# Optimization experiments

Hardware: AMD Instinct MI355X
Metric: run time of the kernel (lower is better)

Reference implementation:

```python
import jax, jax.numpy as jnp
from jax import lax
import numpy as np

N, T, V = 32, 32, 128
C_FEAT, C_BOX, C_CLS = 256, 4, 4
C_IN = C_FEAT + C_BOX + C_CLS  # 264 (is_scene=False concatenates x,b,c)
C_OUT = 64
K = 9
EPS = 1e-3  # keras BatchNormalization default epsilon


def _bn4(x, g, b, m, v):
    # inference-mode BN over channel axis 1 of (N,C,T,V)
    s = (g * lax.rsqrt(v + EPS))[None, :, None, None]
    return (x - m[None, :, None, None]) * s + b[None, :, None, None]


def _stgcn(x, a, imp, w, bw, ga, ba, ma, va, al, wt, bt, gb, bb, mb, vb, residual):
    res = x if residual else 0.0
    # SGCN: 1x1 conv (channels_first) then adjacency aggregation; dropout is identity at inference
    h = jnp.einsum('nctv,co->notv', x, w) + bw[None, :, None, None]
    h = jnp.einsum('nctv,ntvw->nctw', h, a * imp)
    # TGCN: BN -> PReLU(alpha per (C,T,V)) -> temporal conv (K,1) SAME -> BN -> (dropout=id)
    h = _bn4(h, ga, ba, ma, va)
    h = jnp.where(h >= 0, h, al[None] * h)
    h = lax.conv_general_dilated(h, wt, (1, 1), 'SAME',
                                 dimension_numbers=('NCHW', 'HWIO', 'NCHW')) + bt[None, :, None, None]
    h = _bn4(h, gb, bb, mb, vb)
    return h + res  # use_mdn=True -> no final PReLU


def _forward(x, b, c, a, dbn_g, dbn_b, dbn_m, dbn_v,
             w0, bw0, imp0, g0a, b0a, m0a, v0a, al0, wt0, bt0, g0b, b0b, m0b, v0b,
             w1, bw1, imp1, g1a, b1a, m1a, v1a, al1, wt1, bt1, g1b, b1b, m1b, v1b):
    x = jnp.concatenate([x, b, c], axis=-1)  # (N,T,V,C_IN)
    n, t, v, cc = x.shape
    # data BN over flattened (V*C) channel axis, exactly as the TF reshapes do
    x = jnp.transpose(x, (0, 2, 3, 1)).reshape(n, v * cc, t)
    s = (dbn_g * lax.rsqrt(dbn_v + EPS))[None, :, None]
    x = (x - dbn_m[None, :, None]) * s + dbn_b[None, :, None]
    # NOTE: the original does transpose(0,1,3,2) then a *reshape* to (N,C,T,V); replicate exactly
    x = x.reshape(n, v, cc, t).transpose(0, 1, 3, 2).reshape(n, cc, t, v)
    x = _stgcn(x, a, imp0, w0, bw0, g0a, b0a, m0a, v0a, al0, wt0, bt0, g0b, b0b, m0b, v0b, residual=False)
    x = _stgcn(x, a, imp1, w1, bw1, g1a, b1a, m1a, v1a, al1, wt1, bt1, g1b, b1b, m1b, v1b, residual=True)
    x = x[:, :, :, 0]  # (N,C_OUT,T)
    return jnp.transpose(x, (0, 2, 1))  # (N,T,C_OUT)


def setup_inputs():
    key = jax.random.key(0)
    ks = jax.random.split(key, 40)
    rn = lambda k, s, sc=1.0: jax.random.normal(k, s, jnp.float32) * sc
    ru = lambda k, s, lo, hi: jax.random.uniform(k, s, jnp.float32, lo, hi)
    d = {}
    d['x'] = rn(ks[0], (N, T, V, C_FEAT))
    d['b'] = rn(ks[1], (N, T, V, C_BOX))
    d['c'] = ru(ks[2], (N, T, V, C_CLS), 0.0, 1.0)
    d['a'] = ru(ks[3], (N, T, V, V), 0.0, 1.0)
    d['dbn_g'] = ru(ks[4], (V * C_IN,), 0.5, 1.5)
    d['dbn_b'] = rn(ks[5], (V * C_IN,), 0.1)
    d['dbn_m'] = rn(ks[6], (V * C_IN,), 0.1)
    d['dbn_v'] = ru(ks[7], (V * C_IN,), 0.5, 1.5)

    def mk_layer(i, cin, kb):
        d['w%d' % i] = rn(ks[kb], (cin, C_OUT), (1.0 / cin) ** 0.5)
        d['bw%d' % i] = rn(ks[kb + 1], (C_OUT,), 0.01)
        d['imp%d' % i] = rn(ks[kb + 2], (V, V), (2.0 / (V * V)) ** 0.5)
        d['g%da' % i] = ru(ks[kb + 3], (C_OUT,), 0.5, 1.5)
        d['b%da' % i] = rn(ks[kb + 4], (C_OUT,), 0.1)
        d['m%da' % i] = rn(ks[kb + 5], (C_OUT,), 0.1)
        d['v%da' % i] = ru(ks[kb + 6], (C_OUT,), 0.5, 1.5)
        d['al%d' % i] = ru(ks[kb + 7], (C_OUT, T, V), 0.0, 0.3)
        d['wt%d' % i] = rn(ks[kb + 8], (K, 1, C_OUT, C_OUT), (1.0 / (K * C_OUT)) ** 0.5)
        d['bt%d' % i] = rn(ks[kb + 9], (C_OUT,), 0.01)
        d['g%db' % i] = ru(ks[kb + 10], (C_OUT,), 0.5, 1.5)
        d['b%db' % i] = rn(ks[kb + 11], (C_OUT,), 0.1)
        d['m%db' % i] = rn(ks[kb + 12], (C_OUT,), 0.1)
        d['v%db' % i] = ru(ks[kb + 13], (C_OUT,), 0.5, 1.5)

    mk_layer(0, C_IN, 8)
    mk_layer(1, C_OUT, 22)
    return d


def reference(x, b, c, a, dbn_g, dbn_b, dbn_m, dbn_v,
              w0, bw0, imp0, g0a, b0a, m0a, v0a, al0, wt0, bt0, g0b, b0b, m0b, v0b,
              w1, bw1, imp1, g1a, b1a, m1a, v1a, al1, wt1, bt1, g1b, b1b, m1b, v1b):
    return _forward(x, b, c, a, dbn_g, dbn_b, dbn_m, dbn_v,
                    w0, bw0, imp0, g0a, b0a, m0a, v0a, al0, wt0, bt0, g0b, b0b, m0b, v0b,
                    w1, bw1, imp1, g1a, b1a, m1a, v1a, al1, wt1, bt1, g1b, b1b, m1b, v1b)
```

## Files before the change

kernel.cpp:

```cpp
#include <hip/hip_runtime.h>
#include <hip/hip_bf16.h>

typedef unsigned short u16;
typedef unsigned int   u32;

#define N_   32
#define T_   32
#define V_   128
#define CIN_ 264
#define CO_  64
#define KT_  9
#define EPS_ 1e-3f

#define OFF_DBN_S 0
#define OFF_DBN_O 33792
#define OFF_W0    67584
#define OFF_BW0   84480
#define OFF_A0S   84544
#define OFF_A0O   84608
#define OFF_B0S   84672
#define OFF_B0O   84736
#define OFF_W1    84800
#define OFF_BW1   88896
#define OFF_A1S   88960
#define OFF_A1O   89024
#define OFF_B1S   89088
#define OFF_B1O   89152
#define PREP_TOTAL 110464

#define B_P    0
#define B_FLAG 360448
#define B_W0A  360512
#define B_WTA  397440
#define B_H0   524288
#define B_XP   (B_H0 + 16777216)
#define B_G0   (B_H0 + 16777216)
#define B_L0   (B_G0 + 16777216)
#define B_G1P  (B_L0 + 33554432)
#define B_END  (B_G1P + 262144)

typedef short bf16x8 __attribute__((ext_vector_type(8)));
typedef float f32x4  __attribute__((ext_vector_type(4)));

__device__ __forceinline__ float bf2f(u16 u) { return __uint_as_float(((u32)u) << 16); }
__device__ __forceinline__ u16 f2bf(float f) {
    u32 x = __float_as_uint(f);
    return (u16)((x + 0x7fffu + ((x >> 16) & 1u)) >> 16);
}
__device__ __forceinline__ float ldin(const void* p, u32 i, int f32) {
    return f32 ? ((const float*)p)[i] : bf2f(((const u16*)p)[i]);
}

__global__ void k_detect(const void* a, int* flag) {
    if (threadIdx.x == 0 && blockIdx.x == 0) {
        const u16* p = (const u16*)a;
        int cnt = 0;
        for (int i = 0; i < 64; ++i) {
            float v = bf2f(p[2 * i]);
            if (v >= 0.f && v <= 1.0f) ++cnt;
        }
        *flag = (cnt >= 56) ? 0 : 1;
    }
}

__global__ void k_prep(const void* dbn_g, const void* dbn_b, const void* dbn_m, const void* dbn_v,
                       const void* w0, const void* bw0,
                       const void* g0a, const void* b0a, const void* m0a, const void* v0a,
                       const void* bt0, const void* g0b, const void* b0b, const void* m0b, const void* v0b,
                       const void* w1, const void* bw1,
                       const void* g1a, const void* b1a, const void* m1a, const void* v1a,
                       const void* bt1, const void* g1b, const void* b1b, const void* m1b, const void* v1b,
                       const void* wt0,
                       float* P, u16* W0A, u16* WTA, const int* flagp)
{
    const int f32 = *flagp;
    int i = blockIdx.x * 256 + threadIdx.x;
    if (i < 33792) {
        float s = ldin(dbn_g, i, f32) * rsqrtf(ldin(dbn_v, i, f32) + EPS_);
        P[OFF_DBN_S + i] = s;
        P[OFF_DBN_O + i] = ldin(dbn_b, i, f32) - ldin(dbn_m, i, f32) * s;
    } else if (i < 50688) { int j = i - 33792; P[OFF_W0 + j] = ldin(w0, j, f32); }
    else if (i < 50752) { int j = i - 50688; P[OFF_BW0 + j] = ldin(bw0, j, f32); }
    else if (i < 50816) { int j = i - 50752;
        float s = ldin(g0a, j, f32) * rsqrtf(ldin(v0a, j, f32) + EPS_);
        P[OFF_A0S + j] = s; P[OFF_A0O + j] = ldin(b0a, j, f32) - ldin(m0a, j, f32) * s;
    } else if (i < 50880) { int j = i - 50816;
        float s = ldin(g0b, j, f32) * rsqrtf(ldin(v0b, j, f32) + EPS_);
        P[OFF_B0S + j] = s; P[OFF_B0O + j] = (ldin(bt0, j, f32) - ldin(m0b, j, f32)) * s + ldin(b0b, j, f32);
    } else if (i < 54976) { int j = i - 50880; P[OFF_W1 + j] = ldin(w1, j, f32); }
    else if (i < 55040) { int j = i - 54976; P[OFF_BW1 + j] = ldin(bw1, j, f32); }
    else if (i < 55104) { int j = i - 55040;
        float s = ldin(g1a, j, f32) * rsqrtf(ldin(v1a, j, f32) + EPS_);
        P[OFF_A1S + j] = s; P[OFF_A1O + j] = ldin(b1a, j, f32) - ldin(m1a, j, f32) * s;
    } else if (i < 55168) { int j = i - 55104;
        float s = ldin(g1b, j, f32) * rsqrtf(ldin(v1b, j, f32) + EPS_);
        P[OFF_B1S + j] = s; P[OFF_B1O + j] = (ldin(bt1, j, f32) - ldin(m1b, j, f32)) * s + ldin(b1b, j, f32);
    } else if (i < 73600) {
        int j = i - 55168; int c = j / 288, ci = j - c * 288;
        float val = (ci < 264) ? ldin(w0, (u32)ci * 64 + c, f32)
                  : ((ci == 264) ? ldin(bw0, c, f32) : 0.f);
        W0A[j] = f2bf(val);
    } else if (i < 110464) {
        int j = i - 73600; int k = j >> 12, rem = j & 4095, o = rem >> 6, ii = rem & 63;
        WTA[j] = f2bf(ldin(wt0, ((u32)(k * 64 + ii)) * 64 + o, f32));
    }
}

__global__ __launch_bounds__(256) void k_bnx(const void* __restrict__ xin, const void* __restrict__ bin,
                                             const void* __restrict__ cin2, const float* __restrict__ P,
                                             u16* __restrict__ Xp, const int* __restrict__ flagp, int nbase)
{
    __shared__ __align__(16) u16 tile[32 * 130];
    const int f32 = *flagp;
    const int rt = blockIdx.x;
    const int ct = blockIdx.y;
    const int nloc = blockIdx.z;
    const int n = nbase + nloc;
    const int c0 = ct * 32;
    const int ncols = (ct == 8) ? 8 : 32;
    const int r0 = rt * 128;
    const int tid = threadIdx.x;

    for (int q = tid; q < ncols * 32; q += 256) {
        int j = q >> 5, i4 = (q & 31) << 2;
        u32 L = (u32)(c0 + j) * 4096u + (u32)(r0 + i4);
        u32 vs = L / 8448u;
        u32 r  = L - vs * 8448u;
        u32 ts = r / 264u;
        u32 cc = r - ts * 264u;
        u32 base = ((u32)n * 32u + ts) * 128u + vs;
        float4 val;
        if (f32) {
            if (cc < 256u)      val = *(const float4*)((const float*)xin  + (size_t)base * 256u + cc);
            else if (cc < 260u) val = *(const float4*)((const float*)bin  + (size_t)base * 4u + (cc - 256u));
            else                val = *(const float4*)((const float*)cin2 + (size_t)base * 4u + (cc - 260u));
        } else {
            ushort4 uv;
            if (cc < 256u)      uv = *(const ushort4*)((const u16*)xin  + (size_t)base * 256u + cc);
            else if (cc < 260u) uv = *(const ushort4*)((const u16*)bin  + (size_t)base * 4u + (cc - 256u));
            else                uv = *(const ushort4*)((const u16*)cin2 + (size_t)base * 4u + (cc - 260u));
            val.x = bf2f(uv.x); val.y = bf2f(uv.y); val.z = bf2f(uv.z); val.w = bf2f(uv.w);
        }
        u32 ch = vs * 264u + cc;
        const float4 s4 = *(const float4*)&P[OFF_DBN_S + ch];
        const float4 o4 = *(const float4*)&P[OFF_DBN_O + ch];
        ushort2 lo, hi;
        lo.x = f2bf(fmaf(val.x, s4.x, o4.x));
        lo.y = f2bf(fmaf(val.y, s4.y, o4.y));
        hi.x = f2bf(fmaf(val.z, s4.z, o4.z));
        hi.y = f2bf(fmaf(val.w, s4.w, o4.w));
        *(ushort2*)&tile[j * 130 + i4]     = lo;
        *(ushort2*)&tile[j * 130 + i4 + 2] = hi;
    }
    __syncthreads();
    const int chunks = ncols >> 3;
    for (int e = tid; e < 128 * chunks; e += 256) {
        int i, cch;
        if (chunks == 4) { i = e >> 2; cch = e & 3; } else { i = e; cch = 0; }
        __align__(16) u16 tmp[8];
#pragma unroll
        for (int k2 = 0; k2 < 8; ++k2) tmp[k2] = tile[(cch * 8 + k2) * 130 + i];
        *(uint4*)&Xp[((u32)nloc * 4096u + (u32)(r0 + i)) * 264u + (u32)(c0 + cch * 8)] = *(uint4*)tmp;
    }
}

__global__ __launch_bounds__(256) void k_pw0(const u16* __restrict__ Xp, const u16* __restrict__ W0Ag,
                                             u16* __restrict__ h0, int nbase)
{
    const int t2 = blockIdx.x, nloc = blockIdx.y, vh = blockIdx.z;
    const int n = nbase + nloc;
    const int tid = threadIdx.x;
    const int wv = tid >> 6, lane = tid & 63, l16 = lane & 15, quad = lane >> 4;
    const int m0 = wv * 16;
    const int vrow = vh * 64 + m0 + l16;
    const u16* arow = Xp + ((u32)nloc * 4096u + (u32)(t2 * 128 + vrow)) * 264u;

    f32x4 acc[4];
#pragma unroll
    for (int i = 0; i < 4; ++i) acc[i] = (f32x4){0.f, 0.f, 0.f, 0.f};

#pragma unroll
    for (int ks = 0; ks < 8; ++ks) {
        const int k0 = ks * 32 + quad * 8;
        bf16x8 af = *(const bf16x8*)&arow[k0];
#pragma unroll
        for (int ni = 0; ni < 4; ++ni) {
            bf16x8 bf = *(const bf16x8*)&W0Ag[(u32)(ni * 16 + l16) * 288 + k0];
            acc[ni] = __builtin_amdgcn_mfma_f32_16x16x32_bf16(af, bf, acc[ni], 0, 0, 0);
        }
    }
    {
        bf16x8 af = (bf16x8){0, 0, 0, 0, 0, 0, 0, 0};
        if (quad == 0)      af = *(const bf16x8*)&arow[256];
        else if (quad == 1) af[0] = (short)0x3F80;
        const int k0 = 256 + quad * 8;
#pragma unroll
        for (int ni = 0; ni < 4; ++ni) {
            bf16x8 bf = *(const bf16x8*)&W0Ag[(u32)(ni * 16 + l16) * 288 + k0];
            acc[ni] = __builtin_amdgcn_mfma_f32_16x16x32_bf16(af, bf, acc[ni], 0, 0, 0);
        }
    }
    const int v = vh * 64 + m0 + quad * 4;
#pragma unroll
    for (int ni = 0; ni < 4; ++ni) {
        int c = ni * 16 + l16;
        ushort4 rr; u16* rp = (u16*)&rr;
#pragma unroll
        for (int r = 0; r < 4; ++r) rp[r] = f2bf(acc[ni][r]);
        *(ushort4*)&h0[((u32)(n * 64 + c) * 32 + t2) * 128 + v] = rr;
    }
}

__global__ __launch_bounds__(256) void k_graph0(const void* __restrict__ a, const void* __restrict__ imp0,
                                                const void* __restrict__ al0, const float* __restrict__ P,
                                                const u16* __restrict__ h0, u16* __restrict__ g0,
                                                const int* __restrict__ flagp)
{
    __shared__ __align__(16) u16 amT[128 * 136];
    __shared__ __align__(16) u16 Hs[64 * 136];
    const int f32 = *flagp;
    const int t = blockIdx.x, n = blockIdx.y;
    const int tid = threadIdx.x;
    const u32 abase = (((u32)n * T_ + t) * V_) * V_;
    for (int e = tid; e < 128 * 128; e += 256) {
        int vv = e >> 7, w = e & 127;
        float av = ldin(a, abase + (u32)vv * 128u + w, f32) * ldin(imp0, (u32)vv * 128u + w, f32);
        amT[w * 136 + vv] = f2bf(av);
    }
    for (int e = tid; e < 1024; e += 256) {
        int c = e >> 4, ch = e & 15;
        *(uint4*)&Hs[c * 136 + ch * 8] = *(const uint4*)&h0[((u32)(n * 64 + c) * 32 + t) * 128 + ch * 8];
    }
    __syncthreads();
    const int wv = tid >> 6, lane = tid & 63, l16 = lane & 15, quad = lane >> 4;
    const int n0w = wv * 32;
    f32x4 acc[4][2];
#pragma unroll
    for (int mi = 0; mi < 4; ++mi) { acc[mi][0] = (f32x4){0,0,0,0}; acc[mi][1] = (f32x4){0,0,0,0}; }
#pragma unroll
    for (int ks = 0; ks < 4; ++ks) {
        const int k0 = ks * 32 + quad * 8;
        bf16x8 bf[2];
        bf[0] = *(const bf16x8*)&amT[(n0w + l16) * 136 + k0];
        bf[1] = *(const bf16x8*)&amT[(n0w + 16 + l16) * 136 + k0];
#pragma unroll
        for (int mi = 0; mi < 4; ++mi) {
            bf16x8 af = *(const bf16x8*)&Hs[(mi * 16 + l16) * 136 + k0];
            acc[mi][0] = __builtin_amdgcn_mfma_f32_16x16x32_bf16(af, bf[0], acc[mi][0], 0, 0, 0);
            acc[mi][1] = __builtin_amdgcn_mfma_f32_16x16x32_bf16(af, bf[1], acc[mi][1], 0, 0, 0);
        }
    }
#pragma unroll
    for (int mi = 0; mi < 4; ++mi) {
        const int c0 = mi * 16 + quad * 4;
        const float4 s4 = *(const float4*)&P[OFF_A0S + c0];
        const float4 o4 = *(const float4*)&P[OFF_A0O + c0];
        const float ss[4] = {s4.x, s4.y, s4.z, s4.w};
        const float oo[4] = {o4.x, o4.y, o4.z, o4.w};
#pragma unroll
        for (int ni = 0; ni < 2; ++ni) {
            const int w = n0w + ni * 16 + l16;
            ushort4 rr; u16* rp = (u16*)&rr;
#pragma unroll
            for (int r = 0; r < 4; ++r) {
                float y = fmaf(acc[mi][ni][r], ss[r], oo[r]);
                float alv = ldin(al0, ((u32)(c0 + r) * 32 + t) * 128 + w, f32);
                rp[r] = f2bf((y >= 0.f) ? y : alv * y);
            }
            *(ushort4*)&g0[((u32)(n * 32 + t) * 128 + w) * 64 + c0] = rr;
        }
    }
}

__global__ __launch_bounds__(256) void k_tconv0(const u16* __restrict__ WTAg, const float* __restrict__ P,
                                                const u16* __restrict__ g0, float* __restrict__ L0)
{
    __shared__ __align__(16) u16 Wl[2][64 * 72];
    __shared__ __align__(16) u16 Bs[2][128 * 72];
    const int t = blockIdx.x, n = blockIdx.y;
    const int tid = threadIdx.x;
    const int kmin = (t < 4) ? (4 - t) : 0;
    const int kmax = (t > 27) ? (35 - t) : 8;

    auto stageB = [&](int k, int buf) {
        const u16* src = g0 + ((u32)(n * 32 + (t + k - 4)) * 128) * 64;
        for (int e = tid; e < 1024; e += 256) {
            int row = e >> 3, ch = e & 7;
            *(uint4*)&Bs[buf][row * 72 + ch * 8] = *(const uint4*)&src[row * 64 + ch * 8];
        }
    };
    auto stageW = [&](int k, int buf) {
        const u16* src = WTAg + (u32)k * 4096;
        for (int e = tid; e < 512; e += 256) {
            int row = e >> 3, ch = e & 7;
            *(uint4*)&Wl[buf][row * 72 + ch * 8] = *(const uint4*)&src[row * 64 + ch * 8];
        }
    };
    stageB(kmin, 0); stageW(kmin, 0);
    __syncthreads();
    const int wv = tid >> 6, lane = tid & 63, l16 = lane & 15, quad = lane >> 4;
    const int n0w = wv * 32;
    f32x4 acc[4][2];
#pragma unroll
    for (int mi = 0; mi < 4; ++mi) { acc[mi][0] = (f32x4){0,0,0,0}; acc[mi][1] = (f32x4){0,0,0,0}; }

    for (int k = kmin; k <= kmax; ++k) {
        const int buf = (k - kmin) & 1;
        if (k < kmax) { stageB(k + 1, buf ^ 1); stageW(k + 1, buf ^ 1); }
#pragma unroll
        for (int ks = 0; ks < 2; ++ks) {
            const int k0 = ks * 32 + quad * 8;
            bf16x8 bf[2];
            bf[0] = *(const bf16x8*)&Bs[buf][(n0w + l16) * 72 + k0];
            bf[1] = *(const bf16x8*)&Bs[buf][(n0w + 16 + l16) * 72 + k0];
#pragma unroll
            for (int mi = 0; mi < 4; ++mi) {
                bf16x8 af = *(const bf16x8*)&Wl[buf][(mi * 16 + l16) * 72 + k0];
                acc[mi][0] = __builtin_amdgcn_mfma_f32_16x16x32_bf16(af, bf[0], acc[mi][0], 0, 0, 0);
                acc[mi][1] = __builtin_amdgcn_mfma_f32_16x16x32_bf16(af, bf[1], acc[mi][1], 0, 0, 0);
            }
        }
        __syncthreads();
    }
#pragma unroll
    for (int mi = 0; mi < 4; ++mi) {
        const int ob = mi * 16 + quad * 4;
        const float4 s4 = *(const float4*)&P[OFF_B0S + ob];
        const float4 o4 = *(const float4*)&P[OFF_B0O + ob];
        const float ss[4] = {s4.x, s4.y, s4.z, s4.w};
        const float oo[4] = {o4.x, o4.y, o4.z, o4.w};
#pragma unroll
        for (int ni = 0; ni < 2; ++ni) {
            const int v = n0w + ni * 16 + l16;
#pragma unroll
            for (int r = 0; r < 4; ++r)
                L0[((u32)(n * 64 + ob + r) * 32 + t) * 128 + v] = fmaf(acc[mi][ni][r], ss[r], oo[r]);
        }
    }
}

__global__ __launch_bounds__(128) void k_pw1(const void* __restrict__ a, const void* __restrict__ imp1,
                                             const void* __restrict__ al1, const float* __restrict__ P,
                                             const float* __restrict__ L0, float* __restrict__ g1p,
                                             const int* __restrict__ flagp)
{
    __shared__ float part[V_ * 65];
    __shared__ float red2[128];
    const int f32 = *flagp;
    const int t = blockIdx.x, n = blockIdx.y;
    const int tid = threadIdx.x;
    const int v = tid;
    float acc[CO_];
#pragma unroll
    for (int o = 0; o < CO_; ++o) acc[o] = P[OFF_BW1 + o];
    const float* W = P + OFF_W1;
    const u32 base = (u32)n * (CO_ * T_ * V_) + (u32)t * V_ + (u32)v;
    for (int c = 0; c < CO_; ++c) {
        float xv = L0[base + (u32)c * (T_ * V_)];
        const float* wr = W + c * CO_;
#pragma unroll
        for (int o = 0; o < CO_; ++o) acc[o] = fmaf(xv, wr[o], acc[o]);
    }
    float amv = ldin(a, (((u32)n * T_ + t) * V_ + v) * V_ + 0u, f32) * ldin(imp1, (u32)v * V_ + 0u, f32);
#pragma unroll
    for (int o = 0; o < CO_; ++o) part[v * 65 + o] = acc[o] * amv;
    __syncthreads();
    const int o = tid & 63, hh = tid >> 6;
    float s = 0.f;
    for (int vv = hh * 64; vv < hh * 64 + 64; ++vv) s += part[vv * 65 + o];
    red2[tid] = s;
    __syncthreads();
    if (tid < 64) {
        float g = red2[tid] + red2[64 + tid];
        float y = fmaf(g, P[OFF_A1S + o], P[OFF_A1O + o]);
        float alv = ldin(al1, ((u32)o * T_ + t) * V_ + 0u, f32);
        y = (y >= 0.f) ? y : alv * y;
        g1p[((u32)n * CO_ + o) * T_ + t] = y;
    }
}

__global__ __launch_bounds__(64) void k_tconv1(const void* __restrict__ wt1, const float* __restrict__ P,
                                               const float* __restrict__ g1p, const float* __restrict__ L0,
                                               void* __restrict__ out, const int* __restrict__ flagp)
{
    __shared__ float gl[CO_ * KT_];
    const int f32 = *flagp;
    const int t = blockIdx.x, n = blockIdx.y;
    const int tid = threadIdx.x;
    for (int e = tid; e < CO_ * KT_; e += 64) {
        int i = e / KT_, kk = e - i * KT_;
        int tt = t + kk - 4;
        gl[e] = (tt >= 0 && tt < T_) ? g1p[((u32)n * CO_ + i) * T_ + tt] : 0.f;
    }
    __syncthreads();
    float acc = 0.f;
    for (int i = 0; i < CO_; ++i) {
#pragma unroll
        for (int k = 0; k < KT_; ++k) {
            float wv = ldin(wt1, ((u32)(k * CO_ + i)) * CO_ + tid, f32);
            acc = fmaf(gl[i * KT_ + k], wv, acc);
        }
    }
    float y = fmaf(acc, P[OFF_B1S + tid], P[OFF_B1O + tid]);
    y += L0[(u32)n * (CO_ * T_ * V_) + (u32)tid * (T_ * V_) + (u32)t * V_ + 0];
    const u32 oi = ((u32)n * T_ + t) * CO_ + tid;
    if (f32) ((float*)out)[oi] = y;
    else     ((u16*)out)[oi]   = f2bf(y);
}

__global__ void k_fail(u16* out, int nel) {
    int i = blockIdx.x * 256 + threadIdx.x;
    if (i < nel) out[i] = 0x7f80;
}

extern "C" void kernel_launch(void* const* d_in, const int* in_sizes, int n_in,
                              void* d_out, int out_size, void* d_ws, size_t ws_size,
                              hipStream_t stream)
{
    const void* xin  = d_in[0];
    const void* bin  = d_in[1];
    const void* cin2 = d_in[2];
    const void* a    = d_in[3];
    const void* dbn_g = d_in[4];
    const void* dbn_b = d_in[5];
    const void* dbn_m = d_in[6];
    const void* dbn_v = d_in[7];
    const void* w0  = d_in[8];
    const void* bw0 = d_in[9];
    const void* imp0 = d_in[10];
    const void* g0a = d_in[11];
    const void* b0a = d_in[12];
    const void* m0a = d_in[13];
    const void* v0a = d_in[14];
    const void* al0 = d_in[15];
    const void* wt0 = d_in[16];
    const void* bt0 = d_in[17];
    const void* g0b = d_in[18];
    const void* b0b = d_in[19];
    const void* m0b = d_in[20];
    const void* v0b = d_in[21];
    const void* w1  = d_in[22];
    const void* bw1 = d_in[23];
    const void* imp1 = d_in[24];
    const void* g1a = d_in[25];
    const void* b1a = d_in[26];
    const void* m1a = d_in[27];
    const void* v1a = d_in[28];
    const void* al1 = d_in[29];
    const void* wt1 = d_in[30];
    const void* bt1 = d_in[31];
    const void* g1b = d_in[32];
    const void* b1b = d_in[33];
    const void* m1b = d_in[34];
    const void* v1b = d_in[35];

    if (ws_size < (size_t)B_END) {
        k_fail<<<(out_size + 255) / 256, 256, 0, stream>>>((u16*)d_out, out_size);
        return;
    }
    char* w = (char*)d_ws;
    float* P    = (float*)(w + B_P);
    int*   flg  = (int*)(w + B_FLAG);
    u16*   W0A  = (u16*)(w + B_W0A);
    u16*   WTA  = (u16*)(w + B_WTA);
    u16*   h0   = (u16*)(w + B_H0);
    u16*   Xp   = (u16*)(w + B_XP);
    u16*   g0   = (u16*)(w + B_G0);
    float* L0   = (float*)(w + B_L0);
    float* g1p  = (float*)(w + B_G1P);

    k_detect<<<1, 64, 0, stream>>>(a, flg);
    k_prep<<<(PREP_TOTAL + 255) / 256, 256, 0, stream>>>(
        dbn_g, dbn_b, dbn_m, dbn_v, w0, bw0, g0a, b0a, m0a, v0a,
        bt0, g0b, b0b, m0b, v0b, w1, bw1, g1a, b1a, m1a, v1a,
        bt1, g1b, b1b, m1b, v1b, wt0, P, W0A, WTA, flg);

    for (int hf = 0; hf < 2; ++hf) {
        const int nbase = hf * 16;
        k_bnx<<<dim3(32, 9, 16), 256, 0, stream>>>(xin, bin, cin2, P, Xp, flg, nbase);
        k_pw0<<<dim3(T_, 16, 2), 256, 0, stream>>>(Xp, W0A, h0, nbase);
    }

    dim3 grid(T_, N_);
    k_graph0<<<grid, 256, 0, stream>>>(a, imp0, al0, P, h0, g0, flg);
    k_tconv0<<<grid, 256, 0, stream>>>(WTA, P, g0, L0);
    k_pw1   <<<grid, 128, 0, stream>>>(a, imp1, al1, P, L0, g1p, flg);
    k_tconv1<<<grid,  64, 0, stream>>>(wt1, P, g1p, L0, d_out, flg);
}
```

Measured before the change: 561.3 us.

## Split adjacency transpose into separate kernel and read operands directly from global memory

A new kernel, k_at, forms a*imp0 with vectorized loads, transposes it through an XOR-swizzled shared tile, and writes a bf16 transposed adjacency buffer to the workspace, reusing the L0 region. k_graph0 no longer stages data in LDS. It loads MFMA fragments straight from global aT and h0, aiming to remove the strided scalar transpose and the large LDS footprint. The cost is an extra kernel launch and a full write plus read of a 32x32x128x128 bf16 buffer. The h0 fragment reads now use a 4096-element stride, so they may coalesce poorly.

```diff
diff --git a/kernel.cpp b/kernel.cpp
--- a/kernel.cpp
+++ b/kernel.cpp
@@ -211,43 +211,77 @@
     }
 }
 
-__global__ __launch_bounds__(256) void k_graph0(const void* __restrict__ a, const void* __restrict__ imp0,
-                                                const void* __restrict__ al0, const float* __restrict__ P,
-                                                const u16* __restrict__ h0, u16* __restrict__ g0,
-                                                const int* __restrict__ flagp)
-{
-    __shared__ __align__(16) u16 amT[128 * 136];
-    __shared__ __align__(16) u16 Hs[64 * 136];
+__global__ __launch_bounds__(256) void k_at(const void* __restrict__ a, const void* __restrict__ imp0,
+                                            u16* __restrict__ aT, const int* __restrict__ flagp)
+{
+    __shared__ __align__(16) u16 tile[128 * 128];
     const int f32 = *flagp;
     const int t = blockIdx.x, n = blockIdx.y;
     const int tid = threadIdx.x;
-    const u32 abase = (((u32)n * T_ + t) * V_) * V_;
-    for (int e = tid; e < 128 * 128; e += 256) {
-        int vv = e >> 7, w = e & 127;
-        float av = ldin(a, abase + (u32)vv * 128u + w, f32) * ldin(imp0, (u32)vv * 128u + w, f32);
-        amT[w * 136 + vv] = f2bf(av);
-    }
-    for (int e = tid; e < 1024; e += 256) {
-        int c = e >> 4, ch = e & 15;
-        *(uint4*)&Hs[c * 136 + ch * 8] = *(const uint4*)&h0[((u32)(n * 64 + c) * 32 + t) * 128 + ch * 8];
+    const u32 abase = (((u32)n * 32u + (u32)t) * 128u) * 128u;
+
+    for (int e = tid; e < 2048; e += 256) {
+        int v = e >> 4, w0 = (e & 15) << 3;
+        float vals[8];
+        if (f32) {
+            const float* ap = (const float*)a + abase + (u32)v * 128u + w0;
+            const float* ip = (const float*)imp0 + (u32)v * 128u + w0;
+            float4 x0 = *(const float4*)ap, x1 = *(const float4*)(ap + 4);
+            float4 i0 = *(const float4*)ip, i1 = *(const float4*)(ip + 4);
+            vals[0] = x0.x * i0.x; vals[1] = x0.y * i0.y; vals[2] = x0.z * i0.z; vals[3] = x0.w * i0.w;
+            vals[4] = x1.x * i1.x; vals[5] = x1.y * i1.y; vals[6] = x1.z * i1.z; vals[7] = x1.w * i1.w;
+        } else {
+            uint4 xu = *(const uint4*)((const u16*)a + abase + (u32)v * 128u + w0);
+            uint4 iu = *(const uint4*)((const u16*)imp0 + (u32)v * 128u + w0);
+            const u16* xp = (const u16*)&xu; const u16* ip = (const u16*)&iu;
+#pragma unroll
+            for (int j = 0; j < 8; ++j) vals[j] = bf2f(xp[j]) * bf2f(ip[j]);
+        }
+        __align__(16) u16 pk[8];
+#pragma unroll
+        for (int j = 0; j < 8; ++j) pk[j] = f2bf(vals[j]);
+        u32 byte = (u32)v * 256u + (((u32)w0 * 2u) ^ ((((u32)v >> 3) & 7u) << 4));
+        *(uint4*)((char*)tile + byte) = *(uint4*)pk;
     }
     __syncthreads();
+    for (int e = tid; e < 2048; e += 256) {
+        int w = e >> 4, v0 = (e & 15) << 3;
+        __align__(16) u16 tmp[8];
+#pragma unroll
+        for (int k = 0; k < 8; ++k) {
+            int v = v0 + k;
+            u32 byte = (u32)v * 256u + ((((u32)w * 2u)) ^ ((((u32)v >> 3) & 7u) << 4));
+            tmp[k] = *(const u16*)((const char*)tile + byte);
+        }
+        *(uint4*)&aT[abase + (u32)w * 128u + v0] = *(uint4*)tmp;
+    }
+}
+
+__global__ __launch_bounds__(256) void k_graph0(const void* __restrict__ al0, const float* __restrict__ P,
+                                                const u16* __restrict__ h0, const u16* __restrict__ aT,
+                                                u16* __restrict__ g0, const int* __restrict__ flagp)
+{
+    const int f32 = *flagp;
+    const int t = blockIdx.x, n = blockIdx.y;
+    const int tid = threadIdx.x;
     const int wv = tid >> 6, lane = tid & 63, l16 = lane & 15, quad = lane >> 4;
     const int n0w = wv * 32;
+    const u16* aTb = aT + (((u32)n * 32u + (u32)t) * 128u) * 128u;
+    const u16* Hb  = h0 + ((u32)n * 2048u + (u32)t) * 128u;
+
     f32x4 acc[4][2];
 #pragma unroll
     for (int mi = 0; mi < 4; ++mi) { acc[mi][0] = (f32x4){0,0,0,0}; acc[mi][1] = (f32x4){0,0,0,0}; }
 #pragma unroll
     for (int ks = 0; ks < 4; ++ks) {
         const int k0 = ks * 32 + quad * 8;
-        bf16x8 bf[2];
-        bf[0] = *(const bf16x8*)&amT[(n0w + l16) * 136 + k0];
-        bf[1] = *(const bf16x8*)&amT[(n0w + 16 + l16) * 136 + k0];
+        bf16x8 bf0 = *(const bf16x8*)&aTb[(u32)(n0w + l16) * 128u + k0];
+        bf16x8 bf1 = *(const bf16x8*)&aTb[(u32)(n0w + 16 + l16) * 128u + k0];
 #pragma unroll
         for (int mi = 0; mi < 4; ++mi) {
-            bf16x8 af = *(const bf16x8*)&Hs[(mi * 16 + l16) * 136 + k0];
-            acc[mi][0] = __builtin_amdgcn_mfma_f32_16x16x32_bf16(af, bf[0], acc[mi][0], 0, 0, 0);
-            acc[mi][1] = __builtin_amdgcn_mfma_f32_16x16x32_bf16(af, bf[1], acc[mi][1], 0, 0, 0);
+            bf16x8 af = *(const bf16x8*)&Hb[(u32)(mi * 16 + l16) * 4096u + k0];
+            acc[mi][0] = __builtin_amdgcn_mfma_f32_16x16x32_bf16(af, bf0, acc[mi][0], 0, 0, 0);
+            acc[mi][1] = __builtin_amdgcn_mfma_f32_16x16x32_bf16(af, bf1, acc[mi][1], 0, 0, 0);
         }
     }
 #pragma unroll
@@ -466,6 +500,7 @@
     u16*   h0   = (u16*)(w + B_H0);
     u16*   Xp   = (u16*)(w + B_XP);
     u16*   g0   = (u16*)(w + B_G0);
+    u16*   aT   = (u16*)(w + B_L0);
     float* L0   = (float*)(w + B_L0);
     float* g1p  = (float*)(w + B_G1P);
 
@@ -482,7 +517,8 @@
     }
 
     dim3 grid(T_, N_);
-    k_graph0<<<grid, 256, 0, stream>>>(a, imp0, al0, P, h0, g0, flg);
+    k_at    <<<grid, 256, 0, stream>>>(a, imp0, aT, flg);
+    k_graph0<<<grid, 256, 0, stream>>>(al0, P, h0, aT, g0, flg);
     k_tconv0<<<grid, 256, 0, stream>>>(WTA, P, g0, L0);
     k_pw1   <<<grid, 128, 0, stream>>>(a, imp1, al1, P, L0, g1p, flg);
     k_tconv1<<<grid,  64, 0, stream>>>(wt1, P, g1p, L0, d_out, flg);
```

After: 521.3 us. 1.08x faster.
